# Optimization experiments

Measured on AMD Instinct MI355X. Metric: run time of the kernel, lower is better.

Reference implementation:

```python
import jax, jax.numpy as jnp
import numpy as np

B, S, D, H = 32, 577, 768, 12
DH = D // H
MLP = 4 * D
EPS = 1e-5


def _layernorm(x, g, b):
    m = jnp.mean(x, axis=-1, keepdims=True)
    v = jnp.mean((x - m) ** 2, axis=-1, keepdims=True)
    return (x - m) * jax.lax.rsqrt(v + EPS) * g + b


def setup_inputs() -> dict:
    key = jax.random.key(0)
    ks = jax.random.split(key, 12)
    w = lambda k, shp: (jax.random.normal(k, shp, dtype=jnp.float32) * 0.02)
    return {
        "x": jax.random.normal(ks[0], (B, S, D), dtype=jnp.float32),
        "ln1_g": jnp.ones((D,), jnp.float32), "ln1_b": jnp.zeros((D,), jnp.float32),
        "ln2_g": jnp.ones((D,), jnp.float32), "ln2_b": jnp.zeros((D,), jnp.float32),
        "wq": w(ks[1], (H, DH, DH)), "bq": jnp.zeros((H, DH), jnp.float32),
        "wk": w(ks[2], (H, DH, DH)), "bk": jnp.zeros((H, DH), jnp.float32),
        "wv": w(ks[3], (H, DH, DH)), "bv": jnp.zeros((H, DH), jnp.float32),
        "w1": w(ks[4], (D, MLP)), "b1": jnp.zeros((MLP,), jnp.float32),
        "w2": w(ks[5], (MLP, D)), "b2": jnp.zeros((D,), jnp.float32),
    }


def reference(x, ln1_g, ln1_b, ln2_g, ln2_b, wq, bq, wk, bk, wv, bv, w1, b1, w2, b2):
    b, s, d = x.shape
    xn = _layernorm(x, ln1_g, ln1_b)
    xh = xn.reshape(b, s, H, DH)  # split heads along last dim (as in torch slicing)
    # per-head linear maps, batched over heads: [B,H,S,DH]
    q = jnp.einsum('bshd,hdo->bhso', xh, wq) + bq[:, None, :]
    k = jnp.einsum('bshd,hdo->bhso', xh, wk) + bk[:, None, :]
    v = jnp.einsum('bshd,hdo->bhso', xh, wv) + bv[:, None, :]
    scores = jnp.einsum('bhso,bhto->bhst', q, k) / (DH ** 0.5)
    attn = jax.nn.softmax(scores, axis=-1)  # softmax over keys (torch dim=1 of [S,S])
    o = jnp.einsum('bhst,bhtd->bshd', attn, v).reshape(b, s, d)
    out = x + o
    yn = _layernorm(out, ln2_g, ln2_b)
    h = jax.nn.gelu(yn @ w1 + b1, approximate=False)  # torch GELU default is erf-based
    return out + h @ w2 + b2
```

## Files before the change

### kernel.cpp

```cpp
#include <hip/hip_runtime.h>

#define S_LEN 577
#define SPAD  640
#define DMODEL 768
#define NH 12
#define DHEAD 64
#define MLPD 3072
#define NROWS (32 * 577)
#define MPAD  18688
#define NBH   (32 * 12)
#define LOG2E 1.44269504088896340736f

typedef __attribute__((ext_vector_type(8))) short s8v;
typedef __attribute__((ext_vector_type(4))) float f4v;

#define MFMA16(a, b, c) __builtin_amdgcn_mfma_f32_16x16x32_bf16((a), (b), (c), 0, 0, 0)

__device__ __forceinline__ short f2bf(float f) {
  union { float f; unsigned u; } a; a.f = f;
  unsigned r = a.u + 0x7FFFu + ((a.u >> 16) & 1u);
  return (short)(r >> 16);
}
__device__ __forceinline__ short f2bfF(float f) {
  union { float f; unsigned u; } a; a.f = f;
  return (short)((a.u + 0x8000u) >> 16);
}

__device__ __forceinline__ void gload16(const short* g, const short* l) {
  __builtin_amdgcn_global_load_lds(
      (const __attribute__((address_space(1))) void*)g,
      (__attribute__((address_space(3))) void*)l, 16, 0, 0);
}

__global__ __launch_bounds__(256) void transpose_w(const float* __restrict__ in,
                                                   short* __restrict__ out, int R, int C) {
  __shared__ float tile[32][33];
  int c0 = blockIdx.x * 32, r0 = blockIdx.y * 32;
  int tx = threadIdx.x, ty = threadIdx.y;
  for (int i = ty; i < 32; i += 8) tile[i][tx] = in[(size_t)(r0 + i) * C + c0 + tx];
  __syncthreads();
  for (int i = ty; i < 32; i += 8) out[(size_t)(c0 + i) * R + r0 + tx] = f2bf(tile[tx][i]);
}

__global__ __launch_bounds__(256) void prep_qkv(const float* __restrict__ wq, const float* __restrict__ wk,
                                                const float* __restrict__ wv, short* __restrict__ oq,
                                                short* __restrict__ ok, short* __restrict__ ov) {
  int h = blockIdx.x, t = threadIdx.x;
  const float* src0 = wq + (size_t)h * 4096;
  const float* src1 = wk + (size_t)h * 4096;
  const float* src2 = wv + (size_t)h * 4096;
  short* dst0 = oq + (size_t)h * 4096;
  short* dst1 = ok + (size_t)h * 4096;
  short* dst2 = ov + (size_t)h * 4096;
  for (int i = t; i < 4096; i += 256) {
    int o = i >> 6, d = i & 63;
    dst0[i] = f2bf(src0[d * 64 + o]);
    dst1[i] = f2bf(src1[d * 64 + o]);
    dst2[i] = f2bf(src2[d * 64 + o]);
  }
}

__global__ __launch_bounds__(256) void pad_kv(short* __restrict__ kg, short* __restrict__ vt) {
  int idx = blockIdx.x * 256 + threadIdx.x;
  const int padw = SPAD - S_LEN;
  const int per = DHEAD * padw;
  if (idx >= NBH * per) return;
  int bh = idx / per, r = idx - bh * per;
  int col = r / padw, s = S_LEN + (r - col * padw);
  vt[((size_t)bh * DHEAD + col) * SPAD + s] = 0;
  kg[((size_t)bh * SPAD + s) * DHEAD + col] = 0;
}

__global__ __launch_bounds__(256) void ln_kernel(const float* __restrict__ x, const float* __restrict__ g,
                                                 const float* __restrict__ bta, short* __restrict__ out) {
  int row = blockIdx.x;
  int t = threadIdx.x;
  const float* xr = x + (size_t)row * DMODEL;
  float v0 = xr[t], v1 = xr[t + 256], v2 = xr[t + 512];
  float s = v0 + v1 + v2;
  float s2 = v0 * v0 + v1 * v1 + v2 * v2;
  for (int o = 32; o; o >>= 1) { s += __shfl_down(s, o); s2 += __shfl_down(s2, o); }
  __shared__ float red[8];
  if ((t & 63) == 0) { int w = t >> 6; red[w] = s; red[4 + w] = s2; }
  __syncthreads();
  s = red[0] + red[1] + red[2] + red[3];
  s2 = red[4] + red[5] + red[6] + red[7];
  float m = s * (1.f / DMODEL);
  float rs = rsqrtf(s2 * (1.f / DMODEL) - m * m + 1e-5f);
  short* orow = out + (size_t)row * DMODEL;
  orow[t]       = f2bf((v0 - m) * rs * g[t]       + bta[t]);
  orow[t + 256] = f2bf((v1 - m) * rs * g[t + 256] + bta[t + 256]);
  orow[t + 512] = f2bf((v2 - m) * rs * g[t + 512] + bta[t + 512]);
}

__global__ __launch_bounds__(256) void qkv_kernel(const short* __restrict__ xn,
    const short* __restrict__ wqt, const short* __restrict__ wkt, const short* __restrict__ wvt,
    const float* __restrict__ bq, const float* __restrict__ bk, const float* __restrict__ bv,
    short* __restrict__ qg, short* __restrict__ kg, short* __restrict__ vt) {
  __shared__ __align__(16) short wl[3][64][72];
  int bid = blockIdx.x;
  int h = bid % NH, mt = bid / NH;
  int t = threadIdx.x;
  {
    int o = t >> 2, d0 = (t & 3) * 16;
    const short* s0 = wqt + (size_t)h * 4096 + o * 64 + d0;
    const short* s1 = wkt + (size_t)h * 4096 + o * 64 + d0;
    const short* s2 = wvt + (size_t)h * 4096 + o * 64 + d0;
    *(uint4*)&wl[0][o][d0]     = *(const uint4*)s0;
    *(uint4*)&wl[0][o][d0 + 8] = *(const uint4*)(s0 + 8);
    *(uint4*)&wl[1][o][d0]     = *(const uint4*)s1;
    *(uint4*)&wl[1][o][d0 + 8] = *(const uint4*)(s1 + 8);
    *(uint4*)&wl[2][o][d0]     = *(const uint4*)s2;
    *(uint4*)&wl[2][o][d0 + 8] = *(const uint4*)(s2 + 8);
  }
  __syncthreads();
  int w = t >> 6, l = t & 63, l15 = l & 15, lh = l >> 4;
  int m0 = mt * 64 + w * 16;
  if (m0 >= NROWS) return;
  f4v z = {0.f, 0.f, 0.f, 0.f};
  f4v aq[4], ak[4], av[4];
#pragma unroll
  for (int nt = 0; nt < 4; ++nt) { aq[nt] = z; ak[nt] = z; av[nt] = z; }
  const short* xrow = xn + (size_t)(m0 + l15) * DMODEL + h * DHEAD;
#pragma unroll
  for (int kk = 0; kk < 64; kk += 32) {
    s8v af = *(const s8v*)(xrow + kk + lh * 8);
#pragma unroll
    for (int nt = 0; nt < 4; ++nt) {
      s8v b0 = *(const s8v*)&wl[0][nt * 16 + l15][kk + lh * 8];
      s8v b1 = *(const s8v*)&wl[1][nt * 16 + l15][kk + lh * 8];
      s8v b2 = *(const s8v*)&wl[2][nt * 16 + l15][kk + lh * 8];
      aq[nt] = MFMA16(af, b0, aq[nt]);
      ak[nt] = MFMA16(af, b1, ak[nt]);
      av[nt] = MFMA16(af, b2, av[nt]);
    }
  }
#pragma unroll
  for (int nt = 0; nt < 4; ++nt) {
    int col = nt * 16 + l15;
    float biq = bq[h * DHEAD + col], bik = bk[h * DHEAD + col], biv = bv[h * DHEAD + col];
#pragma unroll
    for (int i = 0; i < 4; ++i) {
      int m = m0 + lh * 4 + i;
      int bb = m / S_LEN;
      int ss = m - bb * S_LEN;
      int bh = bb * NH + h;
      qg[((size_t)bh * S_LEN + ss) * DHEAD + col] = f2bf((aq[nt][i] + biq) * (0.125f * LOG2E));
      kg[((size_t)bh * SPAD + ss) * DHEAD + col]  = f2bf(ak[nt][i] + bik);
      vt[((size_t)bh * DHEAD + col) * SPAD + ss]  = f2bf(av[nt][i] + biv);
    }
  }
}

__global__ __launch_bounds__(64, 2) void attn_kernel(const short* __restrict__ qg, const short* __restrict__ kg,
                                                     const short* __restrict__ vt, const float* __restrict__ x,
                                                     float* __restrict__ outp) {
  __shared__ __align__(16) short Pb[2][64][72];
  int bh = blockIdx.x;
  int qt = blockIdx.y;
  int h = bh % NH, b = bh / NH;
  int l = threadIdx.x & 63, l15 = l & 15, lh = l >> 4;
  int q0 = qt * 64;
  size_t qbase = (size_t)bh * S_LEN * DHEAD;
  size_t kbase = (size_t)bh * SPAD * DHEAD;
  size_t vbase = (size_t)bh * DHEAD * SPAD;
  s8v aq[4][2];
#pragma unroll
  for (int f = 0; f < 4; ++f) {
    int qrow = q0 + f * 16 + l15; if (qrow > 576) qrow = 576;
    const short* qp = qg + qbase + (size_t)qrow * DHEAD + lh * 8;
    aq[f][0] = *(const s8v*)qp;
    aq[f][1] = *(const s8v*)(qp + 32);
  }
  f4v z = {0.f, 0.f, 0.f, 0.f};
  f4v z16 = {-16.f, -16.f, -16.f, -16.f};
  f4v acc[4][4];
  float lsum[4][4];
#pragma unroll
  for (int f = 0; f < 4; ++f) {
#pragma unroll
    for (int dt = 0; dt < 4; ++dt) acc[f][dt] = z;
#pragma unroll
    for (int i = 0; i < 4; ++i) lsum[f][i] = 0.f;
  }

  s8v kf0[4], kf1[4], vf[2][4];
  f4v sc[2][4];

#define LOADK(KB)                                                      \
  {                                                                    \
    _Pragma("unroll")                                                  \
    for (int nt = 0; nt < 4; ++nt) {                                   \
      const short* kp = kg + kbase + (size_t)((KB) + nt * 16 + l15) * DHEAD + lh * 8; \
      kf0[nt] = *(const s8v*)kp;                                       \
      kf1[nt] = *(const s8v*)(kp + 32);                                \
    }                                                                  \
  }

#define LOADV(KB)                                                      \
  {                                                                    \
    _Pragma("unroll")                                                  \
    for (int kk2 = 0; kk2 < 2; ++kk2) {                                \
      const short* vp = vt + vbase + (KB) + kk2 * 32 + lh * 8;         \
      _Pragma("unroll")                                                \
      for (int dt = 0; dt < 4; ++dt)                                   \
        vf[kk2][dt] = *(const s8v*)(vp + (size_t)(dt * 16 + l15) * SPAD); \
    }                                                                  \
  }

#define QKT_H(FH)                                                      \
  {                                                                    \
    __builtin_amdgcn_s_setprio(1);                                     \
    _Pragma("unroll")                                                  \
    for (int nt = 0; nt < 4; ++nt) {                                   \
      _Pragma("unroll")                                                \
      for (int fo = 0; fo < 2; ++fo) {                                 \
        f4v a = MFMA16(aq[2 * (FH) + fo][0], kf0[nt], z16);            \
        a = MFMA16(aq[2 * (FH) + fo][1], kf1[nt], a);                  \
        sc[fo][nt] = a;                                                \
      }                                                                \
    }                                                                  \
    __builtin_amdgcn_s_setprio(0);                                     \
  }

#define SMAX_H(FH, PAR, MASK)                                          \
  {                                                                    \
    if (MASK) {                                                        \
      _Pragma("unroll")                                                \
      for (int nt = 0; nt < 4; ++nt) {                                 \
        int col = 576 + nt * 16 + l15;                                 \
        if (col > 576) {                                               \
          _Pragma("unroll")                                            \
          for (int fo = 0; fo < 2; ++fo) {                             \
            sc[fo][nt][0] = sc[fo][nt][1] = sc[fo][nt][2] = sc[fo][nt][3] = -1e30f; } \
        }                                                              \
      }                                                                \
    }                                                                  \
    _Pragma("unroll")                                                  \
    for (int fo = 0; fo < 2; ++fo)                                     \
      _Pragma("unroll")                                                \
      for (int i = 0; i < 4; ++i) {                                    \
        float s = lsum[2 * (FH) + fo][i];                              \
        _Pragma("unroll")                                              \
        for (int nt = 0; nt < 4; ++nt) {                               \
          float e = exp2f(sc[fo][nt][i]);                              \
          s += e;                                                      \
          Pb[PAR][(2 * (FH) + fo) * 16 + lh * 4 + i][nt * 16 + l15] = f2bfF(e); \
        }                                                              \
        lsum[2 * (FH) + fo][i] = s;                                    \
      }                                                                \
  }

#define PVT(PAR)                                                       \
  {                                                                    \
    __builtin_amdgcn_s_setprio(1);                                     \
    _Pragma("unroll")                                                  \
    for (int kk2 = 0; kk2 < 2; ++kk2) {                                \
      _Pragma("unroll")                                                \
      for (int f = 0; f < 4; ++f) {                                    \
        s8v af = *(const s8v*)&Pb[PAR][f * 16 + l15][kk2 * 32 + lh * 8]; \
        _Pragma("unroll")                                              \
        for (int dt = 0; dt < 4; ++dt)                                 \
          acc[f][dt] = MFMA16(af, vf[kk2][dt], acc[f][dt]);            \
      }                                                                \
    }                                                                  \
    __builtin_amdgcn_s_setprio(0);                                     \
  }

  LOADK(0);
  QKT_H(0);
  SMAX_H(0, 0, false);
  QKT_H(1);
  LOADK(64);
  SMAX_H(1, 0, false);

  for (int kt = 0; kt < 10; ++kt) {
    int par = kt & 1;
    LOADV(kt * 64);
    if (kt < 9) {
      bool mask = (kt == 8);
      QKT_H(0);
      SMAX_H(0, par ^ 1, mask);
      QKT_H(1);
      if (kt < 8) LOADK((kt + 2) * 64);
      SMAX_H(1, par ^ 1, mask);
    }
    PVT(par);
  }
#undef LOADK
#undef LOADV
#undef QKT_H
#undef SMAX_H
#undef PVT
#pragma unroll
  for (int f = 0; f < 4; ++f)
#pragma unroll
    for (int i = 0; i < 4; ++i) {
      float s = lsum[f][i];
      s += __shfl_xor(s, 1);
      s += __shfl_xor(s, 2);
      s += __shfl_xor(s, 4);
      s += __shfl_xor(s, 8);
      int srow = q0 + f * 16 + lh * 4 + i;
      if (srow > 576) continue;
      float inv = __builtin_amdgcn_rcpf(s);
      size_t idx0 = ((size_t)b * S_LEN + srow) * DMODEL + h * DHEAD + l15;
#pragma unroll
      for (int dt = 0; dt < 4; ++dt) {
        size_t idx = idx0 + dt * 16;
        outp[idx] = x[idx] + acc[f][dt][i] * inv;
      }
    }
}

#define GEMM32_BODY                                                                \
  int nwg = gridDim.x;                                                             \
  int orig = blockIdx.x;                                                           \
  int qq = nwg >> 3, rr = nwg & 7;                                                 \
  int xcd = orig & 7, lin = orig >> 3;                                             \
  int wg = (xcd < rr ? xcd * (qq + 1) : rr * (qq + 1) + (xcd - rr) * qq) + lin;    \
  int nx = N >> 8;                                                                 \
  int n0 = (wg % nx) * 256, m0 = (wg / nx) * 256;                                  \
  int tid = threadIdx.x;                                                           \
  int wid = tid >> 6, l = tid & 63, l15 = l & 15, lh = l >> 4;                     \
  int wr = wid >> 2, wc = wid & 3;                                                 \
  int srow = tid >> 2, sslot = tid & 3;                                            \
  int scol = (sslot ^ ((srow >> 1) & 3)) * 8;                                      \
  const short* Ab = A + (size_t)m0 * K;                                            \
  const short* Bb = Bt + (size_t)n0 * K;                                           \
  f4v z = {0.f, 0.f, 0.f, 0.f};                                                    \
  f4v acc[4][4];                                                                   \
  _Pragma("unroll") for (int i = 0; i < 4; ++i)                                    \
    _Pragma("unroll") for (int j = 0; j < 4; ++j) acc[i][j] = z;                   \
  s8v af[4], bf[4];                                                                \
  int NT = K >> 5;                                                                 \
  gload16(Ab + (size_t)srow * K + scol, &sA[0][srow][sslot * 8]);                  \
  gload16(Bb + (size_t)srow * K + scol, &sB[0][srow][sslot * 8]);                  \
  int cur = 0;                                                                     \
  for (int kt = 0; kt < NT; ++kt) {                                                \
    __syncthreads();                                                               \
    if (kt + 1 < NT) {                                                             \
      gload16(Ab + (size_t)srow * K + (kt + 1) * 32 + scol, &sA[cur ^ 1][srow][sslot * 8]); \
      gload16(Bb + (size_t)srow * K + (kt + 1) * 32 + scol, &sB[cur ^ 1][srow][sslot * 8]); \
    }                                                                              \
    _Pragma("unroll") for (int mt = 0; mt < 4; ++mt) {                             \
      int r_ = wr * 64 + mt * 16 + l15;                                            \
      af[mt] = *(const s8v*)&sA[cur][r_][(lh ^ ((r_ >> 1) & 3)) * 8];              \
    }                                                                              \
    _Pragma("unroll") for (int nt2 = 0; nt2 < 4; ++nt2) {                          \
      int r_ = wc * 64 + nt2 * 16 + l15;                                           \
      bf[nt2] = *(const s8v*)&sB[cur][r_][(lh ^ ((r_ >> 1) & 3)) * 8];             \
    }                                                                              \
    __builtin_amdgcn_s_setprio(1);                                                 \
    _Pragma("unroll") for (int mt = 0; mt < 4; ++mt)                               \
      _Pragma("unroll") for (int nt2 = 0; nt2 < 4; ++nt2)                          \
        acc[mt][nt2] = MFMA16(af[mt], bf[nt2], acc[mt][nt2]);                      \
    __builtin_amdgcn_s_setprio(0);                                                 \
    cur ^= 1;                                                                      \
  }

__global__ __launch_bounds__(1024) void gemm_gelu(const short* __restrict__ A, const short* __restrict__ Bt,
                                                  const float* __restrict__ bias, short* __restrict__ C,
                                                  int M, int N, int K) {
  __shared__ __align__(16) short sA[2][256][32];
  __shared__ __align__(16) short sB[2][256][32];
  GEMM32_BODY
#pragma unroll
  for (int mt = 0; mt < 4; ++mt)
#pragma unroll
    for (int nt2 = 0; nt2 < 4; ++nt2) {
      int col = n0 + wc * 64 + nt2 * 16 + l15;
      float bi = bias[col];
#pragma unroll
      for (int i = 0; i < 4; ++i) {
        int row = m0 + wr * 64 + mt * 16 + lh * 4 + i;
        float v = acc[mt][nt2][i] + bi;
        float u = v * (2.30221838f + 0.10294364f * v * v);
        v = v * __builtin_amdgcn_rcpf(1.f + exp2f(-u));
        C[(size_t)row * N + col] = f2bfF(v);
      }
    }
}

__global__ __launch_bounds__(1024) void gemm_res(const short* __restrict__ A, const short* __restrict__ Bt,
                                                 const float* __restrict__ bias, float* __restrict__ outp,
                                                 int Mvalid, int N, int K) {
  __shared__ __align__(16) short sA[2][256][32];
  __shared__ __align__(16) short sB[2][256][32];
  GEMM32_BODY
#pragma unroll
  for (int mt = 0; mt < 4; ++mt)
#pragma unroll
    for (int nt2 = 0; nt2 < 4; ++nt2) {
      int col = n0 + wc * 64 + nt2 * 16 + l15;
      float bi = bias[col];
#pragma unroll
      for (int i = 0; i < 4; ++i) {
        int row = m0 + wr * 64 + mt * 16 + lh * 4 + i;
        if (row < Mvalid) {
          size_t idx = (size_t)row * N + col;
          outp[idx] += acc[mt][nt2][i] + bi;
        }
      }
    }
}

extern "C" void kernel_launch(void* const* d_in, const int* in_sizes, int n_in,
                              void* d_out, int out_size, void* d_ws, size_t ws_size,
                              hipStream_t stream) {
  const float* x    = (const float*)d_in[0];
  const float* ln1g = (const float*)d_in[1];
  const float* ln1b = (const float*)d_in[2];
  const float* ln2g = (const float*)d_in[3];
  const float* ln2b = (const float*)d_in[4];
  const float* wq   = (const float*)d_in[5];
  const float* bq   = (const float*)d_in[6];
  const float* wk   = (const float*)d_in[7];
  const float* bk   = (const float*)d_in[8];
  const float* wv   = (const float*)d_in[9];
  const float* bv   = (const float*)d_in[10];
  const float* w1   = (const float*)d_in[11];
  const float* b1   = (const float*)d_in[12];
  const float* w2   = (const float*)d_in[13];
  const float* b2   = (const float*)d_in[14];
  float* outp = (float*)d_out;

  char* ws = (char*)d_ws;
  size_t off = 0;
  auto carve = [&](size_t elems) -> short* {
    short* p = (short*)(ws + off);
    off += elems * sizeof(short);
    off = (off + 255) & ~(size_t)255;
    return p;
  };
  short* yn   = carve((size_t)MPAD * DMODEL);
  short* w1t  = carve((size_t)MLPD * DMODEL);
  short* w2t  = carve((size_t)DMODEL * MLPD);
  short* wqt  = carve((size_t)NH * 64 * 64);
  short* wkt  = carve((size_t)NH * 64 * 64);
  short* wvt  = carve((size_t)NH * 64 * 64);
  size_t union_base = off;
  short* hbuf = carve((size_t)MPAD * MLPD);
  off = union_base;
  short* xn   = carve((size_t)NROWS * DMODEL);
  short* qg   = carve((size_t)NBH * S_LEN * DHEAD);
  short* kg   = carve((size_t)NBH * SPAD * DHEAD);
  short* vtb  = carve((size_t)NBH * DHEAD * SPAD);
  (void)ws_size; (void)in_sizes; (void)n_in; (void)out_size;

  transpose_w<<<dim3(MLPD / 32, DMODEL / 32), dim3(32, 8), 0, stream>>>(w1, w1t, DMODEL, MLPD);
  transpose_w<<<dim3(DMODEL / 32, MLPD / 32), dim3(32, 8), 0, stream>>>(w2, w2t, MLPD, DMODEL);
  prep_qkv<<<NH, 256, 0, stream>>>(wq, wk, wv, wqt, wkt, wvt);
  pad_kv<<<(NBH * DHEAD * (SPAD - S_LEN) + 255) / 256, 256, 0, stream>>>(kg, vtb);

  ln_kernel<<<NROWS, 256, 0, stream>>>(x, ln1g, ln1b, xn);

  qkv_kernel<<<((NROWS + 63) / 64) * NH, 256, 0, stream>>>(xn, wqt, wkt, wvt, bq, bk, bv, qg, kg, vtb);

  attn_kernel<<<dim3(NBH, 10), 64, 0, stream>>>(qg, kg, vtb, x, outp);

  ln_kernel<<<NROWS, 256, 0, stream>>>(outp, ln2g, ln2b, yn);

  gemm_gelu<<<dim3((MPAD / 256) * (MLPD / 256)), 1024, 0, stream>>>(yn, w1t, b1, hbuf, MPAD, MLPD, DMODEL);
  gemm_res<<<dim3((MPAD / 256) * (DMODEL / 256)), 1024, 0, stream>>>(hbuf, w2t, b2, outp, NROWS, DMODEL, MLPD);
}
```

Before: 448.4 us.

## Replace LDS-tiled MLP GEMMs with direct global-to-register double-buffered loads

Both MLP GEMMs drop the shared-memory staging and block-level barriers. Each wave now loads its MFMA fragments straight from global memory into registers, double-buffered over K. Blocks shrink from 1024 to 256 threads with 256x64 tiles, which removes LDS traffic and syncs. The cost is that tiles are no longer shared through LDS, so global/L2 traffic per FLOP rises sharply and the 16-byte per-lane loads with a row stride of K are poorly coalesced.

```diff
diff --git a/kernel.cpp b/kernel.cpp
--- a/kernel.cpp
+++ b/kernel.cpp
@@ -313,67 +313,69 @@
     }
 }
 
-#define GEMM32_BODY                                                                \
+#define GEMMD_BODY                                                                 \
   int nwg = gridDim.x;                                                             \
   int orig = blockIdx.x;                                                           \
   int qq = nwg >> 3, rr = nwg & 7;                                                 \
   int xcd = orig & 7, lin = orig >> 3;                                             \
   int wg = (xcd < rr ? xcd * (qq + 1) : rr * (qq + 1) + (xcd - rr) * qq) + lin;    \
-  int nx = N >> 8;                                                                 \
-  int n0 = (wg % nx) * 256, m0 = (wg / nx) * 256;                                  \
+  int nx = N >> 6;                                                                 \
+  int n0 = (wg % nx) * 64, mb = (wg / nx) * 256;                                   \
   int tid = threadIdx.x;                                                           \
-  int wid = tid >> 6, l = tid & 63, l15 = l & 15, lh = l >> 4;                     \
-  int wr = wid >> 2, wc = wid & 3;                                                 \
-  int srow = tid >> 2, sslot = tid & 3;                                            \
-  int scol = (sslot ^ ((srow >> 1) & 3)) * 8;                                      \
-  const short* Ab = A + (size_t)m0 * K;                                            \
-  const short* Bb = Bt + (size_t)n0 * K;                                           \
+  int w = tid >> 6, l = tid & 63, l15 = l & 15, lh = l >> 4;                       \
+  int m0 = mb + w * 64;                                                            \
+  const short* ap[4];                                                              \
+  const short* bp[4];                                                              \
+  _Pragma("unroll") for (int i = 0; i < 4; ++i) {                                  \
+    ap[i] = A  + (size_t)(m0 + i * 16 + l15) * K + lh * 8;                         \
+    bp[i] = Bt + (size_t)(n0 + i * 16 + l15) * K + lh * 8;                         \
+  }                                                                                \
   f4v z = {0.f, 0.f, 0.f, 0.f};                                                    \
   f4v acc[4][4];                                                                   \
   _Pragma("unroll") for (int i = 0; i < 4; ++i)                                    \
     _Pragma("unroll") for (int j = 0; j < 4; ++j) acc[i][j] = z;                   \
-  s8v af[4], bf[4];                                                                \
+  s8v a0[4], b0[4], a1[4], b1[4];                                                  \
   int NT = K >> 5;                                                                 \
-  gload16(Ab + (size_t)srow * K + scol, &sA[0][srow][sslot * 8]);                  \
-  gload16(Bb + (size_t)srow * K + scol, &sB[0][srow][sslot * 8]);                  \
-  int cur = 0;                                                                     \
-  for (int kt = 0; kt < NT; ++kt) {                                                \
-    __syncthreads();                                                               \
-    if (kt + 1 < NT) {                                                             \
-      gload16(Ab + (size_t)srow * K + (kt + 1) * 32 + scol, &sA[cur ^ 1][srow][sslot * 8]); \
-      gload16(Bb + (size_t)srow * K + (kt + 1) * 32 + scol, &sB[cur ^ 1][srow][sslot * 8]); \
-    }                                                                              \
-    _Pragma("unroll") for (int mt = 0; mt < 4; ++mt) {                             \
-      int r_ = wr * 64 + mt * 16 + l15;                                            \
-      af[mt] = *(const s8v*)&sA[cur][r_][(lh ^ ((r_ >> 1) & 3)) * 8];              \
-    }                                                                              \
-    _Pragma("unroll") for (int nt2 = 0; nt2 < 4; ++nt2) {                          \
-      int r_ = wc * 64 + nt2 * 16 + l15;                                           \
-      bf[nt2] = *(const s8v*)&sB[cur][r_][(lh ^ ((r_ >> 1) & 3)) * 8];             \
+  _Pragma("unroll") for (int i = 0; i < 4; ++i) {                                  \
+    a0[i] = *(const s8v*)ap[i];                                                    \
+    b0[i] = *(const s8v*)bp[i];                                                    \
+  }                                                                                \
+  for (int kt = 0; kt < NT; kt += 2) {                                             \
+    _Pragma("unroll") for (int i = 0; i < 4; ++i) {                                \
+      a1[i] = *(const s8v*)(ap[i] + (kt + 1) * 32);                                \
+      b1[i] = *(const s8v*)(bp[i] + (kt + 1) * 32);                                \
     }                                                                              \
     __builtin_amdgcn_s_setprio(1);                                                 \
     _Pragma("unroll") for (int mt = 0; mt < 4; ++mt)                               \
       _Pragma("unroll") for (int nt2 = 0; nt2 < 4; ++nt2)                          \
-        acc[mt][nt2] = MFMA16(af[mt], bf[nt2], acc[mt][nt2]);                      \
+        acc[mt][nt2] = MFMA16(a0[mt], b0[nt2], acc[mt][nt2]);                      \
     __builtin_amdgcn_s_setprio(0);                                                 \
-    cur ^= 1;                                                                      \
-  }
-
-__global__ __launch_bounds__(1024) void gemm_gelu(const short* __restrict__ A, const short* __restrict__ Bt,
-                                                  const float* __restrict__ bias, short* __restrict__ C,
-                                                  int M, int N, int K) {
-  __shared__ __align__(16) short sA[2][256][32];
-  __shared__ __align__(16) short sB[2][256][32];
-  GEMM32_BODY
+    if (kt + 2 < NT) {                                                             \
+      _Pragma("unroll") for (int i = 0; i < 4; ++i) {                              \
+        a0[i] = *(const s8v*)(ap[i] + (kt + 2) * 32);                              \
+        b0[i] = *(const s8v*)(bp[i] + (kt + 2) * 32);                              \
+      }                                                                            \
+    }                                                                              \
+    __builtin_amdgcn_s_setprio(1);                                                 \
+    _Pragma("unroll") for (int mt = 0; mt < 4; ++mt)                               \
+      _Pragma("unroll") for (int nt2 = 0; nt2 < 4; ++nt2)                          \
+        acc[mt][nt2] = MFMA16(a1[mt], b1[nt2], acc[mt][nt2]);                      \
+    __builtin_amdgcn_s_setprio(0);                                                 \
+  }
+
+__global__ __launch_bounds__(256) void gemm_gelu(const short* __restrict__ A, const short* __restrict__ Bt,
+                                                 const float* __restrict__ bias, short* __restrict__ C,
+                                                 int M, int N, int K) {
+  GEMMD_BODY
 #pragma unroll
   for (int mt = 0; mt < 4; ++mt)
 #pragma unroll
     for (int nt2 = 0; nt2 < 4; ++nt2) {
-      int col = n0 + wc * 64 + nt2 * 16 + l15;
+      int col = n0 + nt2 * 16 + l15;
       float bi = bias[col];
 #pragma unroll
       for (int i = 0; i < 4; ++i) {
-        int row = m0 + wr * 64 + mt * 16 + lh * 4 + i;
+        int row = m0 + mt * 16 + lh * 4 + i;
         float v = acc[mt][nt2][i] + bi;
         float u = v * (2.30221838f + 0.10294364f * v * v);
         v = v * __builtin_amdgcn_rcpf(1.f + exp2f(-u));
@@ -382,21 +384,19 @@
     }
 }
 
-__global__ __launch_bounds__(1024) void gemm_res(const short* __restrict__ A, const short* __restrict__ Bt,
-                                                 const float* __restrict__ bias, float* __restrict__ outp,
-                                                 int Mvalid, int N, int K) {
-  __shared__ __align__(16) short sA[2][256][32];
-  __shared__ __align__(16) short sB[2][256][32];
-  GEMM32_BODY
+__global__ __launch_bounds__(256) void gemm_res(const short* __restrict__ A, const short* __restrict__ Bt,
+                                                const float* __restrict__ bias, float* __restrict__ outp,
+                                                int Mvalid, int N, int K) {
+  GEMMD_BODY
 #pragma unroll
   for (int mt = 0; mt < 4; ++mt)
 #pragma unroll
     for (int nt2 = 0; nt2 < 4; ++nt2) {
-      int col = n0 + wc * 64 + nt2 * 16 + l15;
+      int col = n0 + nt2 * 16 + l15;
       float bi = bias[col];
 #pragma unroll
       for (int i = 0; i < 4; ++i) {
-        int row = m0 + wr * 64 + mt * 16 + lh * 4 + i;
+        int row = m0 + mt * 16 + lh * 4 + i;
         if (row < Mvalid) {
           size_t idx = (size_t)row * N + col;
           outp[idx] += acc[mt][nt2][i] + bi;
@@ -461,6 +461,6 @@
 
   ln_kernel<<<NROWS, 256, 0, stream>>>(outp, ln2g, ln2b, yn);
 
-  gemm_gelu<<<dim3((MPAD / 256) * (MLPD / 256)), 1024, 0, stream>>>(yn, w1t, b1, hbuf, MPAD, MLPD, DMODEL);
-  gemm_res<<<dim3((MPAD / 256) * (DMODEL / 256)), 1024, 0, stream>>>(hbuf, w2t, b2, outp, NROWS, DMODEL, MLPD);
-}
+  gemm_gelu<<<dim3((MPAD / 256) * (MLPD / 64)), 256, 0, stream>>>(yn, w1t, b1, hbuf, MPAD, MLPD, DMODEL);
+  gemm_res<<<dim3((MPAD / 256) * (DMODEL / 64)), 256, 0, stream>>>(hbuf, w2t, b2, outp, NROWS, DMODEL, MLPD);
+}
```

Result: slower. 873.5 us (+94.8%).
